# Kernel optimization log

Hardware: AMD Instinct MI355X
Metric: run time of the kernel (lower is better)

## Reference

```python
import jax, jax.numpy as jnp
import numpy as np

EPS = 1e-08


def _phi(x, W):
    # Performer-style positive random features for the softmax kernel.
    # x: [..., d], W: [d, m]
    d = x.shape[-1]
    m = W.shape[-1]
    proj = jnp.einsum('...d,dm->...m', x, W) * (d ** -0.25)
    sq = jnp.sum(x * x, axis=-1, keepdims=True) / (2.0 * jnp.sqrt(jnp.float32(d)))
    return jnp.exp(proj - sq) * (m ** -0.5)


def setup_inputs() -> dict:
    key = jax.random.key(0)
    k1, k2, k3 = jax.random.split(key, 3)
    B, L, D = 8, 2048, 512
    K = 4
    m = 256
    content_amp = jax.random.normal(k1, (B, L, D), dtype=jnp.float32)
    style_amp = jax.random.normal(k2, (B, K, L, D), dtype=jnp.float32)
    W = jax.random.normal(k3, (D, m), dtype=jnp.float32)
    return {"content_amp": content_amp, "style_amp": style_amp, "W": W}


def reference(content_amp, style_amp, W):
    B, K, L, D = style_amp.shape
    style_seq = style_amp.reshape(B, K * L, D)          # [B, KL, D]
    phi_q = _phi(content_amp, W)                         # [B, Lq, m]
    phi_k = _phi(style_seq, W)                           # [B, KL, m]
    S = jnp.einsum('bkm,bkd->bmd', phi_k, style_seq)     # [B, m, D]
    Z = jnp.sum(phi_k, axis=1)                           # [B, m]
    num = jnp.einsum('blm,bmd->bld', phi_q, S)           # [B, Lq, D]
    den = jnp.einsum('blm,bm->bl', phi_q, Z)[..., None] + EPS
    f_a = num / den
    amp_updated = content_amp + f_a
    return (amp_updated, f_a)
```

## Files before the change

### kernel.cpp

```cpp
#include <hip/hip_runtime.h>
#include <hip/hip_bf16.h>
#include <math.h>

typedef short  s16x8 __attribute__((ext_vector_type(8)));
typedef float  f32x4 __attribute__((ext_vector_type(4)));

#define DD 512
#define MM 256
#define BB 8
#define LL 2048
#define KLT 8192

#define S1f     0.21022410381342864f
#define INV2SDf 0.02209708691207961f
#define S2f     0.0625f
#define EPSV    1e-8f

__device__ __forceinline__ ushort f2b(float f) {
    __hip_bfloat16 h = __float2bfloat16(f);
    return *reinterpret_cast<ushort*>(&h);
}
__device__ __forceinline__ float b2f(ushort u) {
    union { unsigned u32; float f; } x; x.u32 = ((unsigned)u) << 16; return x.f;
}

__global__ __launch_bounds__(256) void convert_kernel(const float* __restrict__ X,
                                                      ushort* __restrict__ Xb,
                                                      float* __restrict__ Sq) {
    const int t = threadIdx.x;
    const int r = blockIdx.x * 64 + (t >> 2);
    const int q = t & 3;
    const float4* src = (const float4*)(X + (size_t)r * DD + q * 128);
    ushort* dst = Xb + (size_t)r * DD + q * 128;
    float s = 0.f;
#pragma unroll
    for (int i = 0; i < 16; ++i) {
        float4 v0 = src[2 * i], v1 = src[2 * i + 1];
        s += v0.x * v0.x + v0.y * v0.y + v0.z * v0.z + v0.w * v0.w
           + v1.x * v1.x + v1.y * v1.y + v1.z * v1.z + v1.w * v1.w;
        s16x8 o;
        o[0] = (short)f2b(v0.x); o[1] = (short)f2b(v0.y);
        o[2] = (short)f2b(v0.z); o[3] = (short)f2b(v0.w);
        o[4] = (short)f2b(v1.x); o[5] = (short)f2b(v1.y);
        o[6] = (short)f2b(v1.z); o[7] = (short)f2b(v1.w);
        *(s16x8*)(dst + 8 * i) = o;
    }
    s += __shfl_xor(s, 1);
    s += __shfl_xor(s, 2);
    if (q == 0) Sq[r] = s * INV2SDf;
}

__global__ __launch_bounds__(256) void prep_w(const float* __restrict__ W,
                                              ushort* __restrict__ Wt) {
    __shared__ ushort lds[64 * 78];
    const int t = threadIdx.x;
    const int dt = blockIdx.x;
    const int mt = blockIdx.y;
    {
        int r = t >> 2, c0 = (t & 3) * 16;
        const float4* src = (const float4*)(W + (size_t)(dt * 64 + r) * MM + mt * 64 + c0);
#pragma unroll
        for (int i = 0; i < 4; ++i) {
            float4 v = src[i];
            lds[r * 78 + c0 + 4 * i + 0] = f2b(v.x);
            lds[r * 78 + c0 + 4 * i + 1] = f2b(v.y);
            lds[r * 78 + c0 + 4 * i + 2] = f2b(v.z);
            lds[r * 78 + c0 + 4 * i + 3] = f2b(v.w);
        }
    }
    __syncthreads();
    {
        int m = t >> 2, d0 = (t & 3) * 16;
        ushort* dst = Wt + (size_t)(mt * 64 + m) * DD + dt * 64 + d0;
#pragma unroll
        for (int j = 0; j < 16; ++j) dst[j] = lds[(d0 + j) * 78 + m];
    }
}

template <bool BT>
__device__ __forceinline__ void gemm128(const ushort* __restrict__ A, int lda,
                                        const ushort* __restrict__ B, int ldb,
                                        int rowbase, int colbase, int k0, int k1,
                                        ushort* sA, ushort* sB, f32x4 acc[4][4]) {
    const int t = threadIdx.x;
    const int l = t & 63, w = t >> 6;
    const int wr = (w >> 1) * 64, wc = (w & 1) * 64;
    const int fr = l & 15, fg = l >> 4;
    const int srow = t >> 1, shalf = t & 1;

    for (int kk = k0; kk < k1; kk += 32) {
        {
            const ushort* src = A + (size_t)(rowbase + srow) * lda + kk + shalf * 16;
            *(s16x8*)(sA + srow * 40 + shalf * 16)     = *(const s16x8*)(src);
            *(s16x8*)(sA + srow * 40 + shalf * 16 + 8) = *(const s16x8*)(src + 8);
        }
        if (!BT) {
            const ushort* src = B + (size_t)(colbase + srow) * ldb + kk + shalf * 16;
            *(s16x8*)(sB + srow * 40 + shalf * 16)     = *(const s16x8*)(src);
            *(s16x8*)(sB + srow * 40 + shalf * 16 + 8) = *(const s16x8*)(src + 8);
        } else {
            const int kl = t & 31, d0c = (t >> 5) * 16;
            const ushort* src = B + (size_t)(kk + kl) * ldb + colbase + d0c;
            s16x8 v0 = *(const s16x8*)(src);
            s16x8 v1 = *(const s16x8*)(src + 8);
#pragma unroll
            for (int j = 0; j < 8; ++j) sB[(d0c + j) * 40 + kl]     = (ushort)v0[j];
#pragma unroll
            for (int j = 0; j < 8; ++j) sB[(d0c + 8 + j) * 40 + kl] = (ushort)v1[j];
        }
        __syncthreads();
        s16x8 a[4], b[4];
#pragma unroll
        for (int mi = 0; mi < 4; ++mi)
            a[mi] = *(const s16x8*)(sA + (wr + mi * 16 + fr) * 40 + fg * 8);
#pragma unroll
        for (int ni = 0; ni < 4; ++ni)
            b[ni] = *(const s16x8*)(sB + (wc + ni * 16 + fr) * 40 + fg * 8);
#pragma unroll
        for (int mi = 0; mi < 4; ++mi)
#pragma unroll
            for (int ni = 0; ni < 4; ++ni)
                acc[mi][ni] = __builtin_amdgcn_mfma_f32_16x16x32_bf16(
                    a[mi], b[ni], acc[mi][ni], 0, 0, 0);
        __syncthreads();
    }
}

__global__ __launch_bounds__(256) void phikt_gemm(const ushort* __restrict__ Wt,
                                                  const ushort* __restrict__ Sb,
                                                  const float* __restrict__ sqk,
                                                  ushort* __restrict__ PhiKT) {
    __shared__ __align__(16) ushort sA[128 * 40];
    __shared__ __align__(16) ushort sB[128 * 40];
    f32x4 acc[4][4] = {};
    const int rowbase = blockIdx.y * 128;
    const int colbase = blockIdx.x * 128;
    gemm128<false>(Wt, DD, Sb, DD, rowbase, colbase, 0, DD, sA, sB, acc);

    const int t = threadIdx.x, l = t & 63, w = t >> 6;
    const int wr = (w >> 1) * 64, wc = (w & 1) * 64, fr = l & 15, fg = l >> 4;
    const int b = colbase >> 13;
    const int kll_base = colbase & (KLT - 1);
#pragma unroll
    for (int ni = 0; ni < 4; ++ni) {
        const int klg = colbase + wc + ni * 16 + fr;
        const int kll = kll_base + wc + ni * 16 + fr;
        const float sqv = sqk[klg];
#pragma unroll
        for (int mi = 0; mi < 4; ++mi)
#pragma unroll
            for (int rr = 0; rr < 4; ++rr) {
                const int m = rowbase + wr + mi * 16 + fg * 4 + rr;
                float v = __expf(acc[mi][ni][rr] * S1f - sqv) * S2f;
                PhiKT[((size_t)b << 21) + ((size_t)m << 13) + kll] = f2b(v);
            }
    }
}

__global__ __launch_bounds__(256) void phiq_gemm(const ushort* __restrict__ Cb,
                                                 const ushort* __restrict__ Wt,
                                                 const float* __restrict__ sqq,
                                                 ushort* __restrict__ PhiQ) {
    __shared__ __align__(16) ushort sA[128 * 40];
    __shared__ __align__(16) ushort sB[128 * 40];
    f32x4 acc[4][4] = {};
    const int rowbase = blockIdx.x * 128;
    const int colbase = blockIdx.y * 128;
    gemm128<false>(Cb, DD, Wt, DD, rowbase, colbase, 0, DD, sA, sB, acc);

    const int t = threadIdx.x, l = t & 63, w = t >> 6;
    const int wr = (w >> 1) * 64, wc = (w & 1) * 64, fr = l & 15, fg = l >> 4;
#pragma unroll
    for (int mi = 0; mi < 4; ++mi)
#pragma unroll
        for (int rr = 0; rr < 4; ++rr) {
            const int lg = rowbase + wr + mi * 16 + fg * 4 + rr;
            const float sqv = sqq[lg];
#pragma unroll
            for (int ni = 0; ni < 4; ++ni) {
                const int m = colbase + wc + ni * 16 + fr;
                float v = __expf(acc[mi][ni][rr] * S1f - sqv) * S2f;
                PhiQ[(size_t)lg * MM + m] = f2b(v);
            }
        }
}

__global__ __launch_bounds__(256) void s_gemm(const ushort* __restrict__ PhiKT,
                                              const ushort* __restrict__ Sb,
                                              float* __restrict__ S) {
    __shared__ __align__(16) ushort sA[128 * 40];
    __shared__ __align__(16) ushort sB[128 * 40];
    f32x4 acc[4][4] = {};
    const int b = blockIdx.z >> 2, split = blockIdx.z & 3;
    const int rowbase = blockIdx.x * 128;
    const int colbase = blockIdx.y * 128;
    const ushort* A = PhiKT + ((size_t)b << 21);
    const ushort* B = Sb + (size_t)b * KLT * DD;
    gemm128<true>(A, KLT, B, DD, rowbase, colbase, split * 2048, split * 2048 + 2048,
                  sA, sB, acc);

    const int t = threadIdx.x, l = t & 63, w = t >> 6;
    const int wr = (w >> 1) * 64, wc = (w & 1) * 64, fr = l & 15, fg = l >> 4;
#pragma unroll
    for (int mi = 0; mi < 4; ++mi)
#pragma unroll
        for (int ni = 0; ni < 4; ++ni)
#pragma unroll
            for (int rr = 0; rr < 4; ++rr) {
                const int m = rowbase + wr + mi * 16 + fg * 4 + rr;
                const int d = colbase + wc + ni * 16 + fr;
                atomicAdd(&S[((size_t)b * MM + m) * DD + d], acc[mi][ni][rr]);
            }
}

__global__ __launch_bounds__(256) void s_fin(const float* __restrict__ S,
                                             ushort* __restrict__ St) {
    __shared__ ushort lds[64 * 78];
    const int t = threadIdx.x;
    const int mt = blockIdx.x, dt = blockIdx.y, b = blockIdx.z;
    {
        int r = t >> 2, c0 = (t & 3) * 16;
        const float4* src =
            (const float4*)(S + ((size_t)b * MM + mt * 64 + r) * DD + dt * 64 + c0);
#pragma unroll
        for (int i = 0; i < 4; ++i) {
            float4 v = src[i];
            lds[r * 78 + c0 + 4 * i + 0] = f2b(v.x);
            lds[r * 78 + c0 + 4 * i + 1] = f2b(v.y);
            lds[r * 78 + c0 + 4 * i + 2] = f2b(v.z);
            lds[r * 78 + c0 + 4 * i + 3] = f2b(v.w);
        }
    }
    __syncthreads();
    {
        int d = t >> 2, m0 = (t & 3) * 16;
        ushort* dst = St + ((size_t)b * DD + dt * 64 + d) * MM + mt * 64 + m0;
#pragma unroll
        for (int j = 0; j < 16; ++j) dst[j] = lds[(m0 + j) * 78 + d];
    }
}

__global__ __launch_bounds__(256) void z_kernel(const ushort* __restrict__ PhiKT,
                                                float* __restrict__ Z) {
    const int row = blockIdx.x * 4 + (threadIdx.x >> 6);
    const int lane = threadIdx.x & 63;
    const int b = row >> 8, m = row & 255;
    const ushort* p = PhiKT + ((size_t)b << 21) + ((size_t)m << 13);
    float s = 0.f;
#pragma unroll
    for (int i = 0; i < 16; ++i) {
        s16x8 v = *(const s16x8*)(p + (size_t)(i * 64 + lane) * 8);
#pragma unroll
        for (int j = 0; j < 8; ++j) s += b2f((ushort)v[j]);
    }
#pragma unroll
    for (int off = 32; off; off >>= 1) s += __shfl_down(s, off);
    if (lane == 0) Z[row] = s;
}

__global__ __launch_bounds__(256) void den_kernel(const ushort* __restrict__ PhiQ,
                                                  const float* __restrict__ Z,
                                                  float* __restrict__ Den) {
    const int row = blockIdx.x * 4 + (threadIdx.x >> 6);
    const int lane = threadIdx.x & 63;
    const int b = row >> 11;
    typedef short s16x4 __attribute__((ext_vector_type(4)));
    s16x4 q = *(const s16x4*)(PhiQ + (size_t)row * MM + lane * 4);
    float4 z = *(const float4*)(Z + (size_t)b * MM + lane * 4);
    float s = b2f((ushort)q[0]) * z.x + b2f((ushort)q[1]) * z.y +
              b2f((ushort)q[2]) * z.z + b2f((ushort)q[3]) * z.w;
#pragma unroll
    for (int off = 32; off; off >>= 1) s += __shfl_down(s, off);
    if (lane == 0) Den[row] = s;
}

__global__ __launch_bounds__(256) void out_gemm(const ushort* __restrict__ PhiQ,
                                                const ushort* __restrict__ St,
                                                const float* __restrict__ Den,
                                                const float* __restrict__ Content,
                                                float* __restrict__ Amp,
                                                float* __restrict__ Fa) {
    __shared__ __align__(16) ushort sA[128 * 40];
    __shared__ __align__(16) ushort sB[128 * 40];
    f32x4 acc[4][4] = {};
    const int b = blockIdx.z;
    const int rowbase = blockIdx.x * 128;
    const int colbase = blockIdx.y * 128;
    const ushort* A = PhiQ + (size_t)b * LL * MM;
    const ushort* B = St + (size_t)b * DD * MM;
    gemm128<false>(A, MM, B, MM, rowbase, colbase, 0, MM, sA, sB, acc);

    const int t = threadIdx.x, l = t & 63, w = t >> 6;
    const int wr = (w >> 1) * 64, wc = (w & 1) * 64, fr = l & 15, fg = l >> 4;
#pragma unroll
    for (int mi = 0; mi < 4; ++mi)
#pragma unroll
        for (int rr = 0; rr < 4; ++rr) {
            const int lg = b * LL + rowbase + wr + mi * 16 + fg * 4 + rr;
            const float inv = 1.0f / (Den[lg] + EPSV);
#pragma unroll
            for (int ni = 0; ni < 4; ++ni) {
                const int d = colbase + wc + ni * 16 + fr;
                const size_t idx = (size_t)lg * DD + d;
                const float f = acc[mi][ni][rr] * inv;
                Fa[idx] = f;
                Amp[idx] = Content[idx] + f;
            }
        }
}

extern "C" void kernel_launch(void* const* d_in, const int* in_sizes, int n_in,
                              void* d_out, int out_size, void* d_ws, size_t ws_size,
                              hipStream_t stream) {
    const float* content = (const float*)d_in[0];
    const float* style   = (const float*)d_in[1];
    const float* Wm      = (const float*)d_in[2];
    float* amp = (float*)d_out;
    float* fa  = (float*)d_out + (size_t)BB * LL * DD;

    float* wsf   = (float*)d_ws;
    float* Sbuf  = wsf;
    float* sq_k  = Sbuf + (size_t)BB * MM * DD;
    float* sq_q  = sq_k + (size_t)BB * KLT;
    float* Zbuf  = sq_q + (size_t)BB * LL;
    float* den   = Zbuf + (size_t)BB * MM;
    ushort* wsu     = (ushort*)(den + (size_t)BB * LL);
    ushort* style_b = wsu;
    ushort* cont_b  = style_b + (size_t)BB * KLT * DD;
    ushort* Wt      = cont_b + (size_t)BB * LL * DD;
    ushort* phi_kT  = Wt + (size_t)MM * DD;
    ushort* phi_q   = phi_kT + (size_t)BB * MM * KLT;
    ushort* St      = phi_q + (size_t)BB * LL * MM;

    hipMemsetAsync(Sbuf, 0, (size_t)BB * MM * DD * sizeof(float), stream);

    prep_w<<<dim3(8, 4), 256, 0, stream>>>(Wm, Wt);
    convert_kernel<<<(BB * LL) / 64, 256, 0, stream>>>(content, cont_b, sq_q);
    convert_kernel<<<(BB * KLT) / 64, 256, 0, stream>>>(style, style_b, sq_k);

    phikt_gemm<<<dim3((BB * KLT) / 128, MM / 128), 256, 0, stream>>>(Wt, style_b, sq_k, phi_kT);
    phiq_gemm<<<dim3((BB * LL) / 128, MM / 128), 256, 0, stream>>>(cont_b, Wt, sq_q, phi_q);

    z_kernel<<<(BB * MM) / 4, 256, 0, stream>>>(phi_kT, Zbuf);
    s_gemm<<<dim3(MM / 128, DD / 128, BB * 4), 256, 0, stream>>>(phi_kT, style_b, Sbuf);
    s_fin<<<dim3(MM / 64, DD / 64, BB), 256, 0, stream>>>(Sbuf, St);

    den_kernel<<<(BB * LL) / 4, 256, 0, stream>>>(phi_q, Zbuf, den);
    out_gemm<<<dim3(LL / 128, DD / 128, BB), 256, 0, stream>>>(phi_q, St, den, content, amp, fa);
}
```

Before: 465.5 us.

## Pre-transpose style bf16 into output scratch and double S-GEMM split-K

Adds a tiled LDS transpose kernel that writes the bf16 style matrix in D-major layout into the output buffer, used as scratch before it is overwritten. The S GEMM can then load its B operand with contiguous vector loads instead of the scalar transposing LDS stores it used before. The S GEMM split-K factor goes from 4 to 8 to launch more blocks, at the cost of more atomic or partial accumulation. The row conversion kernel is also rewritten to use one wavefront per row with coalesced float4 loads. The extra transpose pass adds about 64MB of traffic in exchange for a cheaper GEMM inner loop.

```diff
diff --git a/kernel.cpp b/kernel.cpp
--- a/kernel.cpp
+++ b/kernel.cpp
@@ -3,6 +3,7 @@
 #include <math.h>
 
 typedef short  s16x8 __attribute__((ext_vector_type(8)));
+typedef short  s16x4 __attribute__((ext_vector_type(4)));
 typedef float  f32x4 __attribute__((ext_vector_type(4)));
 
 #define DD 512
@@ -24,30 +25,27 @@
     union { unsigned u32; float f; } x; x.u32 = ((unsigned)u) << 16; return x.f;
 }
 
-__global__ __launch_bounds__(256) void convert_kernel(const float* __restrict__ X,
-                                                      ushort* __restrict__ Xb,
-                                                      float* __restrict__ Sq) {
-    const int t = threadIdx.x;
-    const int r = blockIdx.x * 64 + (t >> 2);
-    const int q = t & 3;
-    const float4* src = (const float4*)(X + (size_t)r * DD + q * 128);
-    ushort* dst = Xb + (size_t)r * DD + q * 128;
-    float s = 0.f;
-#pragma unroll
-    for (int i = 0; i < 16; ++i) {
-        float4 v0 = src[2 * i], v1 = src[2 * i + 1];
-        s += v0.x * v0.x + v0.y * v0.y + v0.z * v0.z + v0.w * v0.w
-           + v1.x * v1.x + v1.y * v1.y + v1.z * v1.z + v1.w * v1.w;
-        s16x8 o;
-        o[0] = (short)f2b(v0.x); o[1] = (short)f2b(v0.y);
-        o[2] = (short)f2b(v0.z); o[3] = (short)f2b(v0.w);
-        o[4] = (short)f2b(v1.x); o[5] = (short)f2b(v1.y);
-        o[6] = (short)f2b(v1.z); o[7] = (short)f2b(v1.w);
-        *(s16x8*)(dst + 8 * i) = o;
-    }
-    s += __shfl_xor(s, 1);
-    s += __shfl_xor(s, 2);
-    if (q == 0) Sq[r] = s * INV2SDf;
+__global__ __launch_bounds__(256) void convert_rows(const float* __restrict__ X,
+                                                    ushort* __restrict__ Xb,
+                                                    float* __restrict__ Sq) {
+    const int row  = blockIdx.x * 4 + (threadIdx.x >> 6);
+    const int lane = threadIdx.x & 63;
+    const float4* src = (const float4*)(X + (size_t)row * DD);
+    float4 v0 = src[lane];
+    float4 v1 = src[lane + 64];
+    float s = v0.x * v0.x + v0.y * v0.y + v0.z * v0.z + v0.w * v0.w
+            + v1.x * v1.x + v1.y * v1.y + v1.z * v1.z + v1.w * v1.w;
+    s16x4* dst = (s16x4*)(Xb + (size_t)row * DD);
+    s16x4 o0, o1;
+    o0[0] = (short)f2b(v0.x); o0[1] = (short)f2b(v0.y);
+    o0[2] = (short)f2b(v0.z); o0[3] = (short)f2b(v0.w);
+    o1[0] = (short)f2b(v1.x); o1[1] = (short)f2b(v1.y);
+    o1[2] = (short)f2b(v1.z); o1[3] = (short)f2b(v1.w);
+    dst[lane]      = o0;
+    dst[lane + 64] = o1;
+#pragma unroll
+    for (int off = 32; off; off >>= 1) s += __shfl_down(s, off);
+    if (lane == 0) Sq[row] = s * INV2SDf;
 }
 
 __global__ __launch_bounds__(256) void prep_w(const float* __restrict__ W,
@@ -77,7 +75,33 @@
     }
 }
 
-template <bool BT>
+__global__ __launch_bounds__(256) void transpose_k(const ushort* __restrict__ Sb,
+                                                   ushort* __restrict__ StyT) {
+    __shared__ ushort lds[64 * 72];
+    const int t = threadIdx.x;
+    const int klt = blockIdx.x;
+    const int dt  = blockIdx.y;
+    const int b   = blockIdx.z;
+    {
+        int r = t >> 2, c0 = (t & 3) * 16;
+        const ushort* src = Sb + ((size_t)b * KLT + klt * 64 + r) * DD + dt * 64 + c0;
+        *(s16x8*)(lds + r * 72 + c0)     = *(const s16x8*)(src);
+        *(s16x8*)(lds + r * 72 + c0 + 8) = *(const s16x8*)(src + 8);
+    }
+    __syncthreads();
+    {
+        int d = t >> 2, k0 = (t & 3) * 16;
+        s16x8 o0, o1;
+#pragma unroll
+        for (int j = 0; j < 8; ++j) o0[j] = (short)lds[(k0 + j) * 72 + d];
+#pragma unroll
+        for (int j = 0; j < 8; ++j) o1[j] = (short)lds[(k0 + 8 + j) * 72 + d];
+        ushort* dst = StyT + ((size_t)b * DD + dt * 64 + d) * KLT + klt * 64 + k0;
+        *(s16x8*)(dst)     = o0;
+        *(s16x8*)(dst + 8) = o1;
+    }
+}
+
 __device__ __forceinline__ void gemm128(const ushort* __restrict__ A, int lda,
                                         const ushort* __restrict__ B, int ldb,
                                         int rowbase, int colbase, int k0, int k1,
@@ -94,19 +118,10 @@
             *(s16x8*)(sA + srow * 40 + shalf * 16)     = *(const s16x8*)(src);
             *(s16x8*)(sA + srow * 40 + shalf * 16 + 8) = *(const s16x8*)(src + 8);
         }
-        if (!BT) {
+        {
             const ushort* src = B + (size_t)(colbase + srow) * ldb + kk + shalf * 16;
             *(s16x8*)(sB + srow * 40 + shalf * 16)     = *(const s16x8*)(src);
             *(s16x8*)(sB + srow * 40 + shalf * 16 + 8) = *(const s16x8*)(src + 8);
-        } else {
-            const int kl = t & 31, d0c = (t >> 5) * 16;
-            const ushort* src = B + (size_t)(kk + kl) * ldb + colbase + d0c;
-            s16x8 v0 = *(const s16x8*)(src);
-            s16x8 v1 = *(const s16x8*)(src + 8);
-#pragma unroll
-            for (int j = 0; j < 8; ++j) sB[(d0c + j) * 40 + kl]     = (ushort)v0[j];
-#pragma unroll
-            for (int j = 0; j < 8; ++j) sB[(d0c + 8 + j) * 40 + kl] = (ushort)v1[j];
         }
         __syncthreads();
         s16x8 a[4], b[4];
@@ -135,7 +150,7 @@
     f32x4 acc[4][4] = {};
     const int rowbase = blockIdx.y * 128;
     const int colbase = blockIdx.x * 128;
-    gemm128<false>(Wt, DD, Sb, DD, rowbase, colbase, 0, DD, sA, sB, acc);
+    gemm128(Wt, DD, Sb, DD, rowbase, colbase, 0, DD, sA, sB, acc);
 
     const int t = threadIdx.x, l = t & 63, w = t >> 6;
     const int wr = (w >> 1) * 64, wc = (w & 1) * 64, fr = l & 15, fg = l >> 4;
@@ -166,7 +181,7 @@
     f32x4 acc[4][4] = {};
     const int rowbase = blockIdx.x * 128;
     const int colbase = blockIdx.y * 128;
-    gemm128<false>(Cb, DD, Wt, DD, rowbase, colbase, 0, DD, sA, sB, acc);
+    gemm128(Cb, DD, Wt, DD, rowbase, colbase, 0, DD, sA, sB, acc);
 
     const int t = threadIdx.x, l = t & 63, w = t >> 6;
     const int wr = (w >> 1) * 64, wc = (w & 1) * 64, fr = l & 15, fg = l >> 4;
@@ -186,18 +201,18 @@
 }
 
 __global__ __launch_bounds__(256) void s_gemm(const ushort* __restrict__ PhiKT,
-                                              const ushort* __restrict__ Sb,
+                                              const ushort* __restrict__ StyT,
                                               float* __restrict__ S) {
     __shared__ __align__(16) ushort sA[128 * 40];
     __shared__ __align__(16) ushort sB[128 * 40];
     f32x4 acc[4][4] = {};
-    const int b = blockIdx.z >> 2, split = blockIdx.z & 3;
+    const int b = blockIdx.z >> 3, split = blockIdx.z & 7;
     const int rowbase = blockIdx.x * 128;
     const int colbase = blockIdx.y * 128;
     const ushort* A = PhiKT + ((size_t)b << 21);
-    const ushort* B = Sb + (size_t)b * KLT * DD;
-    gemm128<true>(A, KLT, B, DD, rowbase, colbase, split * 2048, split * 2048 + 2048,
-                  sA, sB, acc);
+    const ushort* B = StyT + (size_t)b * DD * KLT;
+    gemm128(A, KLT, B, KLT, rowbase, colbase, split * 1024, split * 1024 + 1024,
+            sA, sB, acc);
 
     const int t = threadIdx.x, l = t & 63, w = t >> 6;
     const int wr = (w >> 1) * 64, wc = (w & 1) * 64, fr = l & 15, fg = l >> 4;
@@ -264,7 +279,6 @@
     const int row = blockIdx.x * 4 + (threadIdx.x >> 6);
     const int lane = threadIdx.x & 63;
     const int b = row >> 11;
-    typedef short s16x4 __attribute__((ext_vector_type(4)));
     s16x4 q = *(const s16x4*)(PhiQ + (size_t)row * MM + lane * 4);
     float4 z = *(const float4*)(Z + (size_t)b * MM + lane * 4);
     float s = b2f((ushort)q[0]) * z.x + b2f((ushort)q[1]) * z.y +
@@ -288,7 +302,7 @@
     const int colbase = blockIdx.y * 128;
     const ushort* A = PhiQ + (size_t)b * LL * MM;
     const ushort* B = St + (size_t)b * DD * MM;
-    gemm128<false>(A, MM, B, MM, rowbase, colbase, 0, MM, sA, sB, acc);
+    gemm128(A, MM, B, MM, rowbase, colbase, 0, MM, sA, sB, acc);
 
     const int t = threadIdx.x, l = t & 63, w = t >> 6;
     const int wr = (w >> 1) * 64, wc = (w & 1) * 64, fr = l & 15, fg = l >> 4;
@@ -317,6 +331,8 @@
     const float* Wm      = (const float*)d_in[2];
     float* amp = (float*)d_out;
     float* fa  = (float*)d_out + (size_t)BB * LL * DD;
+
+    ushort* styleT = (ushort*)d_out;
 
     float* wsf   = (float*)d_ws;
     float* Sbuf  = wsf;
@@ -335,14 +351,16 @@
     hipMemsetAsync(Sbuf, 0, (size_t)BB * MM * DD * sizeof(float), stream);
 
     prep_w<<<dim3(8, 4), 256, 0, stream>>>(Wm, Wt);
-    convert_kernel<<<(BB * LL) / 64, 256, 0, stream>>>(content, cont_b, sq_q);
-    convert_kernel<<<(BB * KLT) / 64, 256, 0, stream>>>(style, style_b, sq_k);
+    convert_rows<<<(BB * LL) / 4, 256, 0, stream>>>(content, cont_b, sq_q);
+    convert_rows<<<(BB * KLT) / 4, 256, 0, stream>>>(style, style_b, sq_k);
 
     phikt_gemm<<<dim3((BB * KLT) / 128, MM / 128), 256, 0, stream>>>(Wt, style_b, sq_k, phi_kT);
     phiq_gemm<<<dim3((BB * LL) / 128, MM / 128), 256, 0, stream>>>(cont_b, Wt, sq_q, phi_q);
 
+    transpose_k<<<dim3(KLT / 64, DD / 64, BB), 256, 0, stream>>>(style_b, styleT);
+
     z_kernel<<<(BB * MM) / 4, 256, 0, stream>>>(phi_kT, Zbuf);
-    s_gemm<<<dim3(MM / 128, DD / 128, BB * 4), 256, 0, stream>>>(phi_kT, style_b, Sbuf);
+    s_gemm<<<dim3(MM / 128, DD / 128, BB * 8), 256, 0, stream>>>(phi_kT, styleT, Sbuf);
     s_fin<<<dim3(MM / 64, DD / 64, BB), 256, 0, stream>>>(Sbuf, St);
 
     den_kernel<<<(BB * LL) / 4, 256, 0, stream>>>(phi_q, Zbuf, den);
```

After: 443.6 us. 4.7% less time.
